# Kernel tuning notes

Measured on AMD Instinct MI355X. Metric: run time of the kernel, lower is better.

## Reference

```python
import jax, jax.numpy as jnp
import numpy as np

B, N, C = 8, 512, 256
HID_E = 32          # edge_pred hidden width
FILTERS = (64, 64, 64)
OUT = 2


def setup_inputs() -> dict:
    key = jax.random.key(0)
    ks = jax.random.split(key, 12)
    s = 0.05
    inp = {
        "x": jax.random.normal(ks[0], (B, N, C), jnp.float32),
        "A": jax.random.uniform(ks[1], (B, N, N), jnp.float32),
        "mask": jnp.ones((B, N), jnp.float32),
        # edge predictor: Linear(2C,32) -> ReLU -> Linear(32,1)
        "ew1": jax.random.normal(ks[2], (2 * C, HID_E), jnp.float32) * s,
        "eb1": jnp.zeros((HID_E,), jnp.float32),
        "ew2": jax.random.normal(ks[3], (HID_E, 1), jnp.float32) * s,
        "eb2": jnp.zeros((1,), jnp.float32),
        # GraphConv stack: Linear(in*n_relations, f) per layer (n_relations=2)
        "gw0": jax.random.normal(ks[4], (2 * C, FILTERS[0]), jnp.float32) * s,
        "gb0": jnp.zeros((FILTERS[0],), jnp.float32),
        "gw1": jax.random.normal(ks[5], (2 * FILTERS[0], FILTERS[1]), jnp.float32) * s,
        "gb1": jnp.zeros((FILTERS[1],), jnp.float32),
        "gw2": jax.random.normal(ks[6], (2 * FILTERS[1], FILTERS[2]), jnp.float32) * s,
        "gb2": jnp.zeros((FILTERS[2],), jnp.float32),
        # final classifier (dropout is identity in eval)
        "fcw": jax.random.normal(ks[7], (FILTERS[2], OUT), jnp.float32) * s,
        "fcb": jnp.zeros((OUT,), jnp.float32),
    }
    return inp


def _laplacian(A):
    # A_hat = A + I ; L = D^-1/2 A_hat D^-1/2 with D from row-sums (dim 1)
    n = A.shape[-1]
    A_hat = A + jnp.eye(n, dtype=A.dtype)
    D = (A_hat.sum(axis=1) + 1e-5) ** -0.5  # [B,N]
    return D[:, :, None] * A_hat * D[:, None, :]


def reference(x, A, mask, ew1, eb1, ew2, eb2, gw0, gb0, gw1, gb1, gw2, gb2, fcw, fcb):
    b, n, c = x.shape
    # edge MLP over all node pairs; first layer split so we never build [B,N,N,2C]
    wa, wb = ew1[:c], ew1[c:]
    xa = x @ wa  # [B,N,32] contribution of node i
    xb = x @ wb  # [B,N,32] contribution of node j
    h = jax.nn.relu(xa[:, :, None, :] + xb[:, None, :, :] + eb1)  # [B,N,N,32]
    e = (h @ ew2)[..., 0] + eb2[0]  # e[b,i,j] = edge_pred([x_i, x_j])
    # symmetrized score: exp(0.5 * (f(i,j) + f(j,i)))
    y = jnp.exp(0.5 * (e + jnp.swapaxes(e, 1, 2)))
    triu = jnp.triu(jnp.ones((n, n), bool), 1)
    valid = (mask[:, :, None] > 0) & (mask[:, None, :] > 0)
    A_pred = jnp.where(triu[None] & valid, y, 0.0)
    A_pred = A_pred + jnp.swapaxes(A_pred, 1, 2)

    # multi-relation GCN stack (relations: input A, predicted A_pred)
    L0 = _laplacian(A)
    L1 = _laplacian(A_pred)
    m = mask[:, :, None]
    h0 = x
    for W, bias in ((gw0, gb0), (gw1, gb1), (gw2, gb2)):
        xh = jnp.concatenate([L0 @ h0, L1 @ h0], axis=-1)  # [B,N,2*f_in]
        h0 = jax.nn.relu((xh @ W + bias) * m)
    g = h0.max(axis=1)  # [B, filters[-1]] global max pool over nodes
    return g @ fcw + fcb  # [B, OUT]
```

## Files before the change

kernel.cpp:

```cpp
#include <hip/hip_runtime.h>
#include <hip/hip_bf16.h>
#include <math.h>

#define NB 8
#define NN 512
#define NC 256
#define HID 32

typedef __attribute__((ext_vector_type(8))) short short8;
typedef __attribute__((ext_vector_type(4))) float float4v;
typedef unsigned short ushort_t;

__device__ __forceinline__ ushort_t f2bf(float x) {
    unsigned u = __float_as_uint(x);
    return (ushort_t)((u + 0x7fffu + ((u >> 16) & 1u)) >> 16);
}
__device__ __forceinline__ float bf2f(ushort_t h) {
    return __uint_as_float(((unsigned)h) << 16);
}

__global__ __launch_bounds__(256) void front_gemms(
    const float* __restrict__ x, const float* __restrict__ ew1,
    const float* __restrict__ eb1, const float* __restrict__ gw0,
    const float* __restrict__ A, ushort_t* __restrict__ Ah,
    float* __restrict__ xab, ushort_t* __restrict__ T0,
    float* __restrict__ dsum, unsigned* __restrict__ gmax, int* __restrict__ done)
{
    __shared__ __align__(16) union {
        struct { float sX[2][32][17]; float sW[2][32][68]; } a;
        struct { float sH[2][32][17]; float sW[2][32][132]; ushort_t sTh[128][24]; } b;
    } u;
    __shared__ float sCol[4][64];
    int t = threadIdx.x;

    if (blockIdx.x < 256) {
        if (blockIdx.x < 16) dsum[(NB * NN) + blockIdx.x * 256 + t] = 0.f;
        if (blockIdx.x == 16) {
            gmax[t] = 0u; gmax[t + 256] = 0u;
            if (t < NB) done[t] = 0;
        }
        int r0 = blockIdx.x * 16;
        int tx = t & 15, ty = t >> 4;
        int xk = (t & 15) * 2, xr = t >> 4;
        int c4 = (t & 15) * 4;
        int whalf = c4 >> 5, wcc = c4 & 31;
        float acc[4] = {0.f, 0.f, 0.f, 0.f};

        float2 rx = *(const float2*)(x + (size_t)(r0 + xr) * NC + xk);
        float4 rw0 = *(const float4*)(ew1 + (size_t)(whalf * NC + xr) * HID + wcc);
        float4 rw1 = *(const float4*)(ew1 + (size_t)(whalf * NC + xr + 16) * HID + wcc);

        for (int k0 = 0; k0 < NC; k0 += 32) {
            int cur = (k0 >> 5) & 1;
            u.a.sX[cur][xk][xr] = rx.x; u.a.sX[cur][xk + 1][xr] = rx.y;
            *(float4*)&u.a.sW[cur][xr][c4] = rw0;
            *(float4*)&u.a.sW[cur][xr + 16][c4] = rw1;
            if (k0 + 32 < NC) {
                rx  = *(const float2*)(x + (size_t)(r0 + xr) * NC + k0 + 32 + xk);
                rw0 = *(const float4*)(ew1 + (size_t)(whalf * NC + k0 + 32 + xr) * HID + wcc);
                rw1 = *(const float4*)(ew1 + (size_t)(whalf * NC + k0 + 32 + xr + 16) * HID + wcc);
            }
            __syncthreads();
#pragma unroll
            for (int k = 0; k < 32; ++k) {
                float a = u.a.sX[cur][k][ty];
                float4 w = *(const float4*)&u.a.sW[cur][k][tx * 4];
                acc[0] = fmaf(a, w.x, acc[0]); acc[1] = fmaf(a, w.y, acc[1]);
                acc[2] = fmaf(a, w.z, acc[2]); acc[3] = fmaf(a, w.w, acc[3]);
            }
        }
        int oc4 = tx * 4;
        float4 o; o.x = acc[0]; o.y = acc[1]; o.z = acc[2]; o.w = acc[3];
        if (oc4 >= 32) {
            o.x += eb1[oc4 - 32]; o.y += eb1[oc4 - 31];
            o.z += eb1[oc4 - 30]; o.w += eb1[oc4 - 29];
        }
        *(float4*)&xab[(size_t)(r0 + ty) * 64 + oc4] = o;
    } else if (blockIdx.x < 512) {
        int r0 = (blockIdx.x - 256) * 16;
        int tx = t & 31, ty = t >> 5;
        int xk = (t & 15) * 2, xr = t >> 4;
        int c4w = (t & 31) * 4;
        int whalf = c4w >> 6, wcc = c4w & 63;
        int wk = t >> 5;
        float acc0[4] = {0.f, 0.f, 0.f, 0.f};
        float acc1[4] = {0.f, 0.f, 0.f, 0.f};

        float2 rx = *(const float2*)(x + (size_t)(r0 + xr) * NC + xk);
        float4 rw[4];
#pragma unroll
        for (int rr = 0; rr < 4; ++rr)
            rw[rr] = *(const float4*)(gw0 + (size_t)(whalf * NC + wk + rr * 8) * 64 + wcc);

        for (int k0 = 0; k0 < NC; k0 += 32) {
            int cur = (k0 >> 5) & 1;
            u.b.sH[cur][xk][xr] = rx.x; u.b.sH[cur][xk + 1][xr] = rx.y;
#pragma unroll
            for (int rr = 0; rr < 4; ++rr)
                *(float4*)&u.b.sW[cur][wk + rr * 8][c4w] = rw[rr];
            if (k0 + 32 < NC) {
                rx = *(const float2*)(x + (size_t)(r0 + xr) * NC + k0 + 32 + xk);
#pragma unroll
                for (int rr = 0; rr < 4; ++rr)
                    rw[rr] = *(const float4*)(gw0 + (size_t)(whalf * NC + k0 + 32 + wk + rr * 8) * 64 + wcc);
            }
            __syncthreads();
#pragma unroll
            for (int k = 0; k < 32; ++k) {
                float a0 = u.b.sH[cur][k][ty * 2];
                float a1 = u.b.sH[cur][k][ty * 2 + 1];
                float4 w = *(const float4*)&u.b.sW[cur][k][tx * 4];
                acc0[0] = fmaf(a0, w.x, acc0[0]); acc0[1] = fmaf(a0, w.y, acc0[1]);
                acc0[2] = fmaf(a0, w.z, acc0[2]); acc0[3] = fmaf(a0, w.w, acc0[3]);
                acc1[0] = fmaf(a1, w.x, acc1[0]); acc1[1] = fmaf(a1, w.y, acc1[1]);
                acc1[2] = fmaf(a1, w.z, acc1[2]); acc1[3] = fmaf(a1, w.w, acc1[3]);
            }
        }
        __syncthreads();
        int c4 = tx * 4;
#pragma unroll
        for (int r = 0; r < 2; ++r) {
            int rl = ty * 2 + r;
            float* ap = (r == 0) ? acc0 : acc1;
#pragma unroll
            for (int n = 0; n < 4; ++n)
                u.b.sTh[c4 + n][rl] = f2bf(ap[n]);
        }
        __syncthreads();
        {
            int c = t & 127, half = t >> 7;
            int bb = r0 >> 9, ibase = r0 & (NN - 1);
            ushort_t* dst = T0 + ((size_t)(bb * 128 + c)) * NN + ibase + half * 8;
            *(short8*)dst = *(const short8*)&u.b.sTh[c][half * 8];
        }
    } else {
        int c = blockIdx.x - 512;
        int b = c >> 3, q = c & 7;
        int col = q * 64 + (t & 63);
        int r0 = t >> 6;
        const float* Ab = A + (size_t)b * NN * NN;
        ushort_t* Hb = Ah + (size_t)b * NN * NN;
        float s = 0.f;
        for (int it = 0; it < 128; ++it) {
            int row = r0 + 4 * it;
            float a = Ab[(size_t)row * NN + col];
            Hb[(size_t)row * NN + col] = f2bf(a);
            s += a;
        }
        sCol[r0][t & 63] = s;
        __syncthreads();
        if (t < 64)
            dsum[b * NN + q * 64 + t] =
                sCol[0][t] + sCol[1][t] + sCol[2][t] + sCol[3][t];
    }
}

__global__ __launch_bounds__(256) void edge_scores(
    const float* __restrict__ xab, const float* __restrict__ ew2,
    const float* __restrict__ eb2, const float* __restrict__ mask,
    ushort_t* __restrict__ APh, float* __restrict__ dsum)
{
    __shared__ __align__(16) float sI[32][68], sJ[32][68];
    __shared__ float sV[32][33];
    int b = blockIdx.z;
    int p = blockIdx.x;
    int X = 0;
    while ((X + 1) * 16 - ((X + 1) * X) / 2 <= p) ++X;
    int Y = X + (p - (X * 16 - (X * (X - 1)) / 2));
    int i0 = X * 32, j0 = Y * 32;
    int t = threadIdx.x;
    int tj = t & 31;

    float4 rW[8];
#pragma unroll
    for (int k4 = 0; k4 < 8; ++k4) rW[k4] = *(const float4*)(ew2 + k4 * 4);
    float eb2v = eb2[0];

    {
        int c4 = (t & 15) * 4;
#pragma unroll
        for (int rr = 0; rr < 2; ++rr) {
            int r = (t >> 4) + rr * 16;
            float4 vi = *(const float4*)(xab + ((size_t)(b * NN + i0 + r)) * 64 + c4);
            float4 vj = *(const float4*)(xab + ((size_t)(b * NN + j0 + r)) * 64 + c4);
            *(float4*)&sI[r][c4] = vi;
            *(float4*)&sJ[r][c4] = vj;
        }
    }
    __syncthreads();

    float rJlo[32], rJhi[32];
#pragma unroll
    for (int k4 = 0; k4 < 8; ++k4) {
        float4 a4 = *(const float4*)&sJ[tj][k4 * 4];
        float4 b4 = *(const float4*)&sJ[tj][32 + k4 * 4];
        rJlo[k4 * 4 + 0] = a4.x; rJlo[k4 * 4 + 1] = a4.y;
        rJlo[k4 * 4 + 2] = a4.z; rJlo[k4 * 4 + 3] = a4.w;
        rJhi[k4 * 4 + 0] = b4.x; rJhi[k4 * 4 + 1] = b4.y;
        rJhi[k4 * 4 + 2] = b4.z; rJhi[k4 * 4 + 3] = b4.w;
    }
    float mj = mask[b * NN + j0 + tj];

#pragma unroll
    for (int pz = 0; pz < 4; ++pz) {
        int ti = (t >> 5) + pz * 8;
        float sij = 0.f, sji = 0.f;
#pragma unroll
        for (int k4 = 0; k4 < 8; ++k4) {
            float4 ia = *(const float4*)&sI[ti][k4 * 4];
            float4 ib = *(const float4*)&sI[ti][32 + k4 * 4];
            float4 wv = rW[k4];
            sij = fmaf(fmaxf(ia.x + rJhi[k4 * 4 + 0], 0.f), wv.x, sij);
            sji = fmaf(fmaxf(rJlo[k4 * 4 + 0] + ib.x, 0.f), wv.x, sji);
            sij = fmaf(fmaxf(ia.y + rJhi[k4 * 4 + 1], 0.f), wv.y, sij);
            sji = fmaf(fmaxf(rJlo[k4 * 4 + 1] + ib.y, 0.f), wv.y, sji);
            sij = fmaf(fmaxf(ia.z + rJhi[k4 * 4 + 2], 0.f), wv.z, sij);
            sji = fmaf(fmaxf(rJlo[k4 * 4 + 2] + ib.z, 0.f), wv.z, sji);
            sij = fmaf(fmaxf(ia.w + rJhi[k4 * 4 + 3], 0.f), wv.w, sij);
            sji = fmaf(fmaxf(rJlo[k4 * 4 + 3] + ib.w, 0.f), wv.w, sji);
        }
        int i = i0 + ti, j = j0 + tj;
        bool ok = (i != j) && (mask[b * NN + i] > 0.f) && (mj > 0.f);
        sV[ti][tj] = ok ? expf(0.5f * (sij + sji) + eb2v) : 0.f;
    }
    __syncthreads();
#pragma unroll
    for (int pz = 0; pz < 4; ++pz) {
        int r = (t >> 5) + pz * 8, c = t & 31;
        size_t o1 = ((size_t)(b * NN + i0 + r)) * NN + j0 + c;
        size_t o2 = ((size_t)(b * NN + j0 + r)) * NN + i0 + c;
        APh[o1] = f2bf(sV[r][c]);
        APh[o2] = f2bf(sV[c][r]);
    }
    if (t < 32) {
        float s = 0.f;
#pragma unroll
        for (int r = 0; r < 32; ++r) s += sV[r][t];
        atomicAdd(&dsum[(NB * NN) + b * NN + j0 + t], s);
    } else if (t < 64 && X != Y) {
        int c = t - 32;
        float s = 0.f;
#pragma unroll
        for (int j = 0; j < 32; ++j) s += sV[c][j];
        atomicAdd(&dsum[(NB * NN) + b * NN + i0 + c], s);
    }
}

__global__ __launch_bounds__(256) void fused_layer(
    const ushort_t* __restrict__ Ah, const ushort_t* __restrict__ APh,
    const ushort_t* __restrict__ Pa, const ushort_t* __restrict__ Pb,
    ushort_t* __restrict__ Qa, ushort_t* __restrict__ Qb,
    const float* __restrict__ dsum, const float* __restrict__ gb,
    const float* __restrict__ mask, const float* __restrict__ gwN,
    unsigned* __restrict__ gmax, int* __restrict__ done,
    const float* __restrict__ fcw, const float* __restrict__ fcb,
    float* __restrict__ out, int dualP, int mode, int scaleP)
{
    __shared__ union {
        struct {
            ushort_t sA[2][2][16][72];
            ushort_t sP1[2][64][72];
            ushort_t sP2[2][64][72];
        } a;
        struct { ushort_t sWT[128][40]; } b;
    } u;
    __shared__ float sRed[2][32][17];
    __shared__ float sH16[16][36];
    __shared__ float sD[2][16];
    __shared__ __align__(16) float sDj[2][NN];
    __shared__ int lastFlag;

    int t = threadIdx.x;
    int b = blockIdx.z, ch = blockIdx.y, i0 = blockIdx.x * 16;
    int lane = t & 63, w = t >> 6;
    int quad = lane >> 4, m16 = lane & 15;
    int lap = w >> 1, cg = w & 1;

    if (scaleP) {
#pragma unroll
        for (int s = 0; s < 4; ++s) {
            int idx = t + s * 256;
            int lp = idx >> 9, j = idx & (NN - 1);
            sDj[lp][j] = rsqrtf(dsum[lp * (NB * NN) + b * NN + j] + 1.0f + 1e-5f);
        }
    }

    int sa_arr = t >> 7, sa_id = t & 127;
    int sa_r = sa_id >> 3, sa_q = sa_id & 7;
    const ushort_t* sa_src = (sa_arr ? APh : Ah)
        + ((size_t)(b * NN + i0 + sa_r)) * NN + sa_q * 8;
    int pl0 = t >> 3, pq = t & 7;
    size_t poff0 = ((size_t)(b * 128 + ch * 32 + pl0)) * NN + pq * 8;
    size_t poff1 = ((size_t)(b * 128 + 64 + ch * 32 + pl0)) * NN + pq * 8;

    int gi = b * NN + i0 + m16;
    float dspre = dsum[lap * (NB * NN) + gi];
    int cbase = cg * 16 + quad * 4;
    size_t pvbase = ((size_t)(b * 128 + lap * 64 + ch * 32 + cbase)) * NN + i0 + m16;
    ushort_t pvA[4], pvB[4];
#pragma unroll
    for (int r = 0; r < 4; ++r) {
        pvA[r] = Pa[pvbase + (size_t)r * NN];
        pvB[r] = dualP ? Pb[pvbase + (size_t)r * NN] : (ushort_t)0;
    }

    float gwPre[16];
    if (mode == 0) {
#pragma unroll
        for (int kk = 0; kk < 8; ++kk) {
            int chunk = t + kk * 256;
            int c = chunk & 127;
            int k = (chunk >> 7) * 2;
            int base = (c < 64) ? (ch * 32) : (64 + ch * 32);
            int gc = c & 63;
            gwPre[kk * 2]     = gwN[(size_t)(base + k) * 64 + gc];
            gwPre[kk * 2 + 1] = gwN[(size_t)(base + k + 1) * 64 + gc];
        }
    }

    float4v acc = {0.f, 0.f, 0.f, 0.f};

    short8 A0, P1a0, P1b0, P2a0, P2b0;
    short8 A1, P1a1, P1b1, P2a1, P2b1;

    A0   = *(const short8*)(sa_src);
    P1a0 = *(const short8*)(Pa + poff0);
    P1b0 = *(const short8*)(Pa + poff1);
    A1   = *(const short8*)(sa_src + 64);
    P1a1 = *(const short8*)(Pa + poff0 + 64);
    P1b1 = *(const short8*)(Pa + poff1 + 64);
    P2a0 = P1a0; P2b0 = P1b0; P2a1 = P1a1; P2b1 = P1b1;
    if (dualP) {
        P2a0 = *(const short8*)(Pb + poff0);
        P2b0 = *(const short8*)(Pb + poff1);
        P2a1 = *(const short8*)(Pb + poff0 + 64);
        P2b1 = *(const short8*)(Pb + poff1 + 64);
    }
    __syncthreads();

#pragma unroll
    for (int i = 0; i < 8; ++i) {
        int k0 = i * 64;
        int cur = i & 1;
        short8 rA   = cur ? A1   : A0;
        short8 rP1a = cur ? P1a1 : P1a0;
        short8 rP1b = cur ? P1b1 : P1b0;
        short8 rP2a = cur ? P2a1 : P2a0;
        short8 rP2b = cur ? P2b1 : P2b0;

        *(short8*)&u.a.sA[cur][sa_arr][sa_r][sa_q * 8] = rA;
        if (scaleP) {
            float4v d0a = *(const float4v*)&sDj[0][k0 + pq * 8];
            float4v d0b = *(const float4v*)&sDj[0][k0 + pq * 8 + 4];
            float4v d1a = *(const float4v*)&sDj[1][k0 + pq * 8];
            float4v d1b = *(const float4v*)&sDj[1][k0 + pq * 8 + 4];
            short8 w0, w1;
#pragma unroll
            for (int e = 0; e < 4; ++e) {
                w0[e]     = (short)f2bf(bf2f((ushort_t)rP1a[e])     * d0a[e]);
                w0[e + 4] = (short)f2bf(bf2f((ushort_t)rP1a[e + 4]) * d0b[e]);
                w1[e]     = (short)f2bf(bf2f((ushort_t)rP1b[e])     * d1a[e]);
                w1[e + 4] = (short)f2bf(bf2f((ushort_t)rP1b[e + 4]) * d1b[e]);
            }
            *(short8*)&u.a.sP1[cur][pl0][pq * 8] = w0;
            *(short8*)&u.a.sP1[cur][32 + pl0][pq * 8] = w1;
        } else {
            *(short8*)&u.a.sP1[cur][pl0][pq * 8] = rP1a;
            *(short8*)&u.a.sP1[cur][32 + pl0][pq * 8] = rP1b;
            if (dualP) {
                *(short8*)&u.a.sP2[cur][pl0][pq * 8] = rP2a;
                *(short8*)&u.a.sP2[cur][32 + pl0][pq * 8] = rP2b;
            }
        }
        if (i + 2 < 8) {
            int kn = k0 + 128;
            if (cur == 0) {
                A0   = *(const short8*)(sa_src + kn);
                P1a0 = *(const short8*)(Pa + poff0 + kn);
                P1b0 = *(const short8*)(Pa + poff1 + kn);
                if (dualP) {
                    P2a0 = *(const short8*)(Pb + poff0 + kn);
                    P2b0 = *(const short8*)(Pb + poff1 + kn);
                }
            } else {
                A1   = *(const short8*)(sa_src + kn);
                P1a1 = *(const short8*)(Pa + poff0 + kn);
                P1b1 = *(const short8*)(Pa + poff1 + kn);
                if (dualP) {
                    P2a1 = *(const short8*)(Pb + poff0 + kn);
                    P2b1 = *(const short8*)(Pb + poff1 + kn);
                }
            }
        }
        __syncthreads();
#pragma unroll
        for (int kh = 0; kh < 2; ++kh) {
            int ko = kh * 32 + quad * 8;
            short8 av = *(const short8*)&u.a.sA[cur][lap][m16][ko];
            short8 p1 = *(const short8*)&u.a.sP1[cur][w * 16 + m16][ko];
            acc = __builtin_amdgcn_mfma_f32_16x16x32_bf16(p1, av, acc, 0, 0, 0);
            if (dualP) {
                short8 p2 = *(const short8*)&u.a.sP2[cur][w * 16 + m16][ko];
                acc = __builtin_amdgcn_mfma_f32_16x16x32_bf16(p2, av, acc, 0, 0, 0);
            }
        }
    }
    float d = rsqrtf(dspre + 1.0f + 1e-5f);
    if (cg == 0 && quad == 0) sD[lap][m16] = d;
#pragma unroll
    for (int r = 0; r < 4; ++r) {
        int c32 = cbase + r;
        float pv = bf2f(pvA[r]);
        if (dualP) pv += bf2f(pvB[r]);
        if (scaleP) pv *= d;
        sRed[lap][c32][m16] = d * (acc[r] + pv);
    }
    __syncthreads();
#pragma unroll
    for (int s = 0; s < 2; ++s) {
        int idx = t + s * 256;
        int c32 = idx & 31, i = idx >> 5;
        float mv = mask[b * NN + i0 + i];
        float v = (sRed[0][c32][i] + sRed[1][c32][i] + gb[ch * 32 + c32]) * mv;
        sH16[i][c32] = fmaxf(v, 0.f);
    }
    __syncthreads();

    if (mode == 0) {
#pragma unroll
        for (int kk = 0; kk < 8; ++kk) {
            int chunk = t + kk * 256;
            int c = chunk & 127;
            int k = (chunk >> 7) * 2;
            unsigned pk = (unsigned)f2bf(gwPre[kk * 2])
                        | ((unsigned)f2bf(gwPre[kk * 2 + 1]) << 16);
            *(unsigned*)&u.b.sWT[c][k] = pk;
        }
        __syncthreads();
        float4 h0 = *(const float4*)&sH16[m16][quad * 8];
        float4 h1 = *(const float4*)&sH16[m16][quad * 8 + 4];
        short8 bfv;
        bfv[0] = f2bf(h0.x); bfv[1] = f2bf(h0.y); bfv[2] = f2bf(h0.z); bfv[3] = f2bf(h0.w);
        bfv[4] = f2bf(h1.x); bfv[5] = f2bf(h1.y); bfv[6] = f2bf(h1.z); bfv[7] = f2bf(h1.w);
        ushort_t* Q = ch ? Qb : Qa;
#pragma unroll
        for (int s2 = 0; s2 < 2; ++s2) {
            int ctile = w * 2 + s2;
            short8 af = *(const short8*)&u.b.sWT[ctile * 16 + m16][quad * 8];
            float4v dacc = {0.f, 0.f, 0.f, 0.f};
            dacc = __builtin_amdgcn_mfma_f32_16x16x32_bf16(af, bfv, dacc, 0, 0, 0);
            float dsc = sD[(ctile >= 4) ? 1 : 0][m16];
#pragma unroll
            for (int r = 0; r < 4; ++r) {
                int c = ctile * 16 + quad * 4 + r;
                Q[((size_t)(b * 128 + c)) * NN + i0 + m16] = f2bf(dsc * dacc[r]);
            }
        }
    } else {
        if (t < 32) {
            float mx = 0.f;
#pragma unroll
            for (int r = 0; r < 16; ++r) mx = fmaxf(mx, sH16[r][t]);
            atomicMax(&gmax[b * 64 + ch * 32 + t], __float_as_uint(mx));
        }
        __syncthreads();
        if (t == 0) {
            __threadfence();
            int old = atomicAdd(&done[b], 1);
            lastFlag = (old == 63);
        }
        __syncthreads();
        if (lastFlag) {
            if (t < 64) {
                unsigned ub = __hip_atomic_load(&gmax[b * 64 + t],
                                                __ATOMIC_RELAXED,
                                                __HIP_MEMORY_SCOPE_AGENT);
                ((float*)sRed)[t] = __uint_as_float(ub);
            }
            __syncthreads();
            if (t < 2) {
                float a2 = fcb[t];
#pragma unroll
                for (int k = 0; k < 64; ++k)
                    a2 = fmaf(((float*)sRed)[k], fcw[k * 2 + t], a2);
                out[b * 2 + t] = a2;
            }
        }
    }
}

extern "C" void kernel_launch(void* const* d_in, const int* in_sizes, int n_in,
                              void* d_out, int out_size, void* d_ws, size_t ws_size,
                              hipStream_t stream)
{
    const float* x    = (const float*)d_in[0];
    const float* A    = (const float*)d_in[1];
    const float* mask = (const float*)d_in[2];
    const float* ew1  = (const float*)d_in[3];
    const float* eb1  = (const float*)d_in[4];
    const float* ew2  = (const float*)d_in[5];
    const float* eb2  = (const float*)d_in[6];
    const float* gw0  = (const float*)d_in[7];
    const float* gb0  = (const float*)d_in[8];
    const float* gw1  = (const float*)d_in[9];
    const float* gb1  = (const float*)d_in[10];
    const float* gw2  = (const float*)d_in[11];
    const float* gb2  = (const float*)d_in[12];
    const float* fcw  = (const float*)d_in[13];
    const float* fcb  = (const float*)d_in[14];
    float* out = (float*)d_out;
    char* ws = (char*)d_ws;

    const size_t NEL = (size_t)NB * NN * NN;
    const size_t PSL = (size_t)NB * 128 * NN;
    float*    xab  = (float*)ws;                   ws += 262144 * 4;
    ushort_t* APh  = (ushort_t*)ws;                ws += NEL * 2;
    ushort_t* Ahs  = (ushort_t*)ws;                ws += NEL * 2;
    float*    dsum = (float*)ws;                   ws += 8192 * 4;
    ushort_t* PT_A = (ushort_t*)ws;                ws += PSL * 2;
    ushort_t* PB1a = (ushort_t*)ws;                ws += PSL * 2;
    ushort_t* PB1b = (ushort_t*)ws;                ws += PSL * 2;
    ushort_t* PB2a = (ushort_t*)ws;                ws += PSL * 2;
    ushort_t* PB2b = (ushort_t*)ws;                ws += PSL * 2;
    unsigned* gmax = (unsigned*)ws;                ws += 512 * 4;
    int*      done = (int*)ws;                     ws += 64 * 4;

    front_gemms<<<576, 256, 0, stream>>>(x, ew1, eb1, gw0, A, Ahs, xab, PT_A,
                                         dsum, gmax, done);
    edge_scores<<<dim3(136, 1, NB), 256, 0, stream>>>(xab, ew2, eb2, mask,
                                                      APh, dsum);

    fused_layer<<<dim3(32, 2, NB), 256, 0, stream>>>(
        Ahs, APh, PT_A, PT_A, PB1a, PB1b, dsum, gb0, mask, gw1,
        gmax, done, fcw, fcb, out, 0, 0, 1);
    fused_layer<<<dim3(32, 2, NB), 256, 0, stream>>>(
        Ahs, APh, PB1a, PB1b, PB2a, PB2b, dsum, gb1, mask, gw2,
        gmax, done, fcw, fcb, out, 1, 0, 0);
    fused_layer<<<dim3(32, 2, NB), 256, 0, stream>>>(
        Ahs, APh, PB2a, PB2b, PB2a, PB2b, dsum, gb2, mask, gw2,
        gmax, done, fcw, fcb, out, 1, 1, 0);
}
```

Measured before the change: 151.2 us.

## Rebalance front kernels so edge scoring runs alongside gw0 GEMM and A conversion

Splits the first kernel so only the xa/xb GEMM (which edge scoring depends on) runs first. The gw0 GEMM, the A-to-bf16 conversion with row sums, and the edge scoring now share one launch of 1408 blocks. The independent work can then overlap instead of sitting behind a dependency boundary. The gw0 GEMM also drops its double-buffered shared memory for a single buffer with an extra barrier, which shrinks the LDS union but serialises load and compute within that path.

```diff
diff --git a/kernel.cpp b/kernel.cpp
--- a/kernel.cpp
+++ b/kernel.cpp
@@ -19,65 +19,76 @@
     return __uint_as_float(((unsigned)h) << 16);
 }
 
-__global__ __launch_bounds__(256) void front_gemms(
+__global__ __launch_bounds__(256) void xaxb_gemm(
     const float* __restrict__ x, const float* __restrict__ ew1,
-    const float* __restrict__ eb1, const float* __restrict__ gw0,
-    const float* __restrict__ A, ushort_t* __restrict__ Ah,
-    float* __restrict__ xab, ushort_t* __restrict__ T0,
+    const float* __restrict__ eb1, float* __restrict__ xab,
     float* __restrict__ dsum, unsigned* __restrict__ gmax, int* __restrict__ done)
 {
+    __shared__ __align__(16) struct { float sX[2][32][17]; float sW[2][32][68]; } u;
+    int t = threadIdx.x;
+
+    if (blockIdx.x < 16) dsum[(NB * NN) + blockIdx.x * 256 + t] = 0.f;
+    if (blockIdx.x == 16) {
+        gmax[t] = 0u; gmax[t + 256] = 0u;
+        if (t < NB) done[t] = 0;
+    }
+    int r0 = blockIdx.x * 16;
+    int tx = t & 15, ty = t >> 4;
+    int xk = (t & 15) * 2, xr = t >> 4;
+    int c4 = (t & 15) * 4;
+    int whalf = c4 >> 5, wcc = c4 & 31;
+    float acc[4] = {0.f, 0.f, 0.f, 0.f};
+
+    float2 rx = *(const float2*)(x + (size_t)(r0 + xr) * NC + xk);
+    float4 rw0 = *(const float4*)(ew1 + (size_t)(whalf * NC + xr) * HID + wcc);
+    float4 rw1 = *(const float4*)(ew1 + (size_t)(whalf * NC + xr + 16) * HID + wcc);
+
+    for (int k0 = 0; k0 < NC; k0 += 32) {
+        int cur = (k0 >> 5) & 1;
+        u.sX[cur][xk][xr] = rx.x; u.sX[cur][xk + 1][xr] = rx.y;
+        *(float4*)&u.sW[cur][xr][c4] = rw0;
+        *(float4*)&u.sW[cur][xr + 16][c4] = rw1;
+        if (k0 + 32 < NC) {
+            rx  = *(const float2*)(x + (size_t)(r0 + xr) * NC + k0 + 32 + xk);
+            rw0 = *(const float4*)(ew1 + (size_t)(whalf * NC + k0 + 32 + xr) * HID + wcc);
+            rw1 = *(const float4*)(ew1 + (size_t)(whalf * NC + k0 + 32 + xr + 16) * HID + wcc);
+        }
+        __syncthreads();
+#pragma unroll
+        for (int k = 0; k < 32; ++k) {
+            float a = u.sX[cur][k][ty];
+            float4 w = *(const float4*)&u.sW[cur][k][tx * 4];
+            acc[0] = fmaf(a, w.x, acc[0]); acc[1] = fmaf(a, w.y, acc[1]);
+            acc[2] = fmaf(a, w.z, acc[2]); acc[3] = fmaf(a, w.w, acc[3]);
+        }
+    }
+    int oc4 = tx * 4;
+    float4 o; o.x = acc[0]; o.y = acc[1]; o.z = acc[2]; o.w = acc[3];
+    if (oc4 >= 32) {
+        o.x += eb1[oc4 - 32]; o.y += eb1[oc4 - 31];
+        o.z += eb1[oc4 - 30]; o.w += eb1[oc4 - 29];
+    }
+    *(float4*)&xab[(size_t)(r0 + ty) * 64 + oc4] = o;
+}
+
+__global__ __launch_bounds__(256) void edge_plus(
+    const float* __restrict__ x, const float* __restrict__ gw0,
+    const float* __restrict__ A, ushort_t* __restrict__ Ah,
+    const float* __restrict__ xab, const float* __restrict__ ew2,
+    const float* __restrict__ eb2, const float* __restrict__ mask,
+    ushort_t* __restrict__ T0, ushort_t* __restrict__ APh,
+    float* __restrict__ dsum)
+{
     __shared__ __align__(16) union {
-        struct { float sX[2][32][17]; float sW[2][32][68]; } a;
-        struct { float sH[2][32][17]; float sW[2][32][132]; ushort_t sTh[128][24]; } b;
+        struct { float sH[32][17]; float sW[32][132]; ushort_t sTh[128][24]; } b;
+        struct { float sI[32][68]; float sJ[32][68]; float sV[32][33]; } e;
     } u;
     __shared__ float sCol[4][64];
+    int bid = blockIdx.x;
     int t = threadIdx.x;
 
-    if (blockIdx.x < 256) {
-        if (blockIdx.x < 16) dsum[(NB * NN) + blockIdx.x * 256 + t] = 0.f;
-        if (blockIdx.x == 16) {
-            gmax[t] = 0u; gmax[t + 256] = 0u;
-            if (t < NB) done[t] = 0;
-        }
-        int r0 = blockIdx.x * 16;
-        int tx = t & 15, ty = t >> 4;
-        int xk = (t & 15) * 2, xr = t >> 4;
-        int c4 = (t & 15) * 4;
-        int whalf = c4 >> 5, wcc = c4 & 31;
-        float acc[4] = {0.f, 0.f, 0.f, 0.f};
-
-        float2 rx = *(const float2*)(x + (size_t)(r0 + xr) * NC + xk);
-        float4 rw0 = *(const float4*)(ew1 + (size_t)(whalf * NC + xr) * HID + wcc);
-        float4 rw1 = *(const float4*)(ew1 + (size_t)(whalf * NC + xr + 16) * HID + wcc);
-
-        for (int k0 = 0; k0 < NC; k0 += 32) {
-            int cur = (k0 >> 5) & 1;
-            u.a.sX[cur][xk][xr] = rx.x; u.a.sX[cur][xk + 1][xr] = rx.y;
-            *(float4*)&u.a.sW[cur][xr][c4] = rw0;
-            *(float4*)&u.a.sW[cur][xr + 16][c4] = rw1;
-            if (k0 + 32 < NC) {
-                rx  = *(const float2*)(x + (size_t)(r0 + xr) * NC + k0 + 32 + xk);
-                rw0 = *(const float4*)(ew1 + (size_t)(whalf * NC + k0 + 32 + xr) * HID + wcc);
-                rw1 = *(const float4*)(ew1 + (size_t)(whalf * NC + k0 + 32 + xr + 16) * HID + wcc);
-            }
-            __syncthreads();
-#pragma unroll
-            for (int k = 0; k < 32; ++k) {
-                float a = u.a.sX[cur][k][ty];
-                float4 w = *(const float4*)&u.a.sW[cur][k][tx * 4];
-                acc[0] = fmaf(a, w.x, acc[0]); acc[1] = fmaf(a, w.y, acc[1]);
-                acc[2] = fmaf(a, w.z, acc[2]); acc[3] = fmaf(a, w.w, acc[3]);
-            }
-        }
-        int oc4 = tx * 4;
-        float4 o; o.x = acc[0]; o.y = acc[1]; o.z = acc[2]; o.w = acc[3];
-        if (oc4 >= 32) {
-            o.x += eb1[oc4 - 32]; o.y += eb1[oc4 - 31];
-            o.z += eb1[oc4 - 30]; o.w += eb1[oc4 - 29];
-        }
-        *(float4*)&xab[(size_t)(r0 + ty) * 64 + oc4] = o;
-    } else if (blockIdx.x < 512) {
-        int r0 = (blockIdx.x - 256) * 16;
+    if (bid < 256) {
+        int r0 = bid * 16;
         int tx = t & 31, ty = t >> 5;
         int xk = (t & 15) * 2, xr = t >> 4;
         int c4w = (t & 31) * 4;
@@ -93,11 +104,10 @@
             rw[rr] = *(const float4*)(gw0 + (size_t)(whalf * NC + wk + rr * 8) * 64 + wcc);
 
         for (int k0 = 0; k0 < NC; k0 += 32) {
-            int cur = (k0 >> 5) & 1;
-            u.b.sH[cur][xk][xr] = rx.x; u.b.sH[cur][xk + 1][xr] = rx.y;
+            u.b.sH[xk][xr] = rx.x; u.b.sH[xk + 1][xr] = rx.y;
 #pragma unroll
             for (int rr = 0; rr < 4; ++rr)
-                *(float4*)&u.b.sW[cur][wk + rr * 8][c4w] = rw[rr];
+                *(float4*)&u.b.sW[wk + rr * 8][c4w] = rw[rr];
             if (k0 + 32 < NC) {
                 rx = *(const float2*)(x + (size_t)(r0 + xr) * NC + k0 + 32 + xk);
 #pragma unroll
@@ -107,16 +117,16 @@
             __syncthreads();
 #pragma unroll
             for (int k = 0; k < 32; ++k) {
-                float a0 = u.b.sH[cur][k][ty * 2];
-                float a1 = u.b.sH[cur][k][ty * 2 + 1];
-                float4 w = *(const float4*)&u.b.sW[cur][k][tx * 4];
+                float a0 = u.b.sH[k][ty * 2];
+                float a1 = u.b.sH[k][ty * 2 + 1];
+                float4 w = *(const float4*)&u.b.sW[k][tx * 4];
                 acc0[0] = fmaf(a0, w.x, acc0[0]); acc0[1] = fmaf(a0, w.y, acc0[1]);
                 acc0[2] = fmaf(a0, w.z, acc0[2]); acc0[3] = fmaf(a0, w.w, acc0[3]);
                 acc1[0] = fmaf(a1, w.x, acc1[0]); acc1[1] = fmaf(a1, w.y, acc1[1]);
                 acc1[2] = fmaf(a1, w.z, acc1[2]); acc1[3] = fmaf(a1, w.w, acc1[3]);
             }
-        }
-        __syncthreads();
+            __syncthreads();
+        }
         int c4 = tx * 4;
 #pragma unroll
         for (int r = 0; r < 2; ++r) {
@@ -133,8 +143,8 @@
             ushort_t* dst = T0 + ((size_t)(bb * 128 + c)) * NN + ibase + half * 8;
             *(short8*)dst = *(const short8*)&u.b.sTh[c][half * 8];
         }
-    } else {
-        int c = blockIdx.x - 512;
+    } else if (bid < 320) {
+        int c = bid - 256;
         int b = c >> 3, q = c & 7;
         int col = q * 64 + (t & 63);
         int r0 = t >> 6;
@@ -152,97 +162,88 @@
         if (t < 64)
             dsum[b * NN + q * 64 + t] =
                 sCol[0][t] + sCol[1][t] + sCol[2][t] + sCol[3][t];
-    }
-}
-
-__global__ __launch_bounds__(256) void edge_scores(
-    const float* __restrict__ xab, const float* __restrict__ ew2,
-    const float* __restrict__ eb2, const float* __restrict__ mask,
-    ushort_t* __restrict__ APh, float* __restrict__ dsum)
-{
-    __shared__ __align__(16) float sI[32][68], sJ[32][68];
-    __shared__ float sV[32][33];
-    int b = blockIdx.z;
-    int p = blockIdx.x;
-    int X = 0;
-    while ((X + 1) * 16 - ((X + 1) * X) / 2 <= p) ++X;
-    int Y = X + (p - (X * 16 - (X * (X - 1)) / 2));
-    int i0 = X * 32, j0 = Y * 32;
-    int t = threadIdx.x;
-    int tj = t & 31;
-
-    float4 rW[8];
-#pragma unroll
-    for (int k4 = 0; k4 < 8; ++k4) rW[k4] = *(const float4*)(ew2 + k4 * 4);
-    float eb2v = eb2[0];
-
-    {
-        int c4 = (t & 15) * 4;
-#pragma unroll
-        for (int rr = 0; rr < 2; ++rr) {
-            int r = (t >> 4) + rr * 16;
-            float4 vi = *(const float4*)(xab + ((size_t)(b * NN + i0 + r)) * 64 + c4);
-            float4 vj = *(const float4*)(xab + ((size_t)(b * NN + j0 + r)) * 64 + c4);
-            *(float4*)&sI[r][c4] = vi;
-            *(float4*)&sJ[r][c4] = vj;
-        }
-    }
-    __syncthreads();
-
-    float rJlo[32], rJhi[32];
-#pragma unroll
-    for (int k4 = 0; k4 < 8; ++k4) {
-        float4 a4 = *(const float4*)&sJ[tj][k4 * 4];
-        float4 b4 = *(const float4*)&sJ[tj][32 + k4 * 4];
-        rJlo[k4 * 4 + 0] = a4.x; rJlo[k4 * 4 + 1] = a4.y;
-        rJlo[k4 * 4 + 2] = a4.z; rJlo[k4 * 4 + 3] = a4.w;
-        rJhi[k4 * 4 + 0] = b4.x; rJhi[k4 * 4 + 1] = b4.y;
-        rJhi[k4 * 4 + 2] = b4.z; rJhi[k4 * 4 + 3] = b4.w;
-    }
-    float mj = mask[b * NN + j0 + tj];
-
-#pragma unroll
-    for (int pz = 0; pz < 4; ++pz) {
-        int ti = (t >> 5) + pz * 8;
-        float sij = 0.f, sji = 0.f;
+    } else {
+        int e0 = bid - 320;
+        int b = e0 / 136, p = e0 - b * 136;
+        int X = 0;
+        while ((X + 1) * 16 - ((X + 1) * X) / 2 <= p) ++X;
+        int Y = X + (p - (X * 16 - (X * (X - 1)) / 2));
+        int i0 = X * 32, j0 = Y * 32;
+        int tj = t & 31;
+
+        float4 rW[8];
+#pragma unroll
+        for (int k4 = 0; k4 < 8; ++k4) rW[k4] = *(const float4*)(ew2 + k4 * 4);
+        float eb2v = eb2[0];
+
+        {
+            int c4 = (t & 15) * 4;
+#pragma unroll
+            for (int rr = 0; rr < 2; ++rr) {
+                int r = (t >> 4) + rr * 16;
+                float4 vi = *(const float4*)(xab + ((size_t)(b * NN + i0 + r)) * 64 + c4);
+                float4 vj = *(const float4*)(xab + ((size_t)(b * NN + j0 + r)) * 64 + c4);
+                *(float4*)&u.e.sI[r][c4] = vi;
+                *(float4*)&u.e.sJ[r][c4] = vj;
+            }
+        }
+        __syncthreads();
+
+        float rJlo[32], rJhi[32];
 #pragma unroll
         for (int k4 = 0; k4 < 8; ++k4) {
-            float4 ia = *(const float4*)&sI[ti][k4 * 4];
-            float4 ib = *(const float4*)&sI[ti][32 + k4 * 4];
-            float4 wv = rW[k4];
-            sij = fmaf(fmaxf(ia.x + rJhi[k4 * 4 + 0], 0.f), wv.x, sij);
-            sji = fmaf(fmaxf(rJlo[k4 * 4 + 0] + ib.x, 0.f), wv.x, sji);
-            sij = fmaf(fmaxf(ia.y + rJhi[k4 * 4 + 1], 0.f), wv.y, sij);
-            sji = fmaf(fmaxf(rJlo[k4 * 4 + 1] + ib.y, 0.f), wv.y, sji);
-            sij = fmaf(fmaxf(ia.z + rJhi[k4 * 4 + 2], 0.f), wv.z, sij);
-            sji = fmaf(fmaxf(rJlo[k4 * 4 + 2] + ib.z, 0.f), wv.z, sji);
-            sij = fmaf(fmaxf(ia.w + rJhi[k4 * 4 + 3], 0.f), wv.w, sij);
-            sji = fmaf(fmaxf(rJlo[k4 * 4 + 3] + ib.w, 0.f), wv.w, sji);
-        }
-        int i = i0 + ti, j = j0 + tj;
-        bool ok = (i != j) && (mask[b * NN + i] > 0.f) && (mj > 0.f);
-        sV[ti][tj] = ok ? expf(0.5f * (sij + sji) + eb2v) : 0.f;
-    }
-    __syncthreads();
-#pragma unroll
-    for (int pz = 0; pz < 4; ++pz) {
-        int r = (t >> 5) + pz * 8, c = t & 31;
-        size_t o1 = ((size_t)(b * NN + i0 + r)) * NN + j0 + c;
-        size_t o2 = ((size_t)(b * NN + j0 + r)) * NN + i0 + c;
-        APh[o1] = f2bf(sV[r][c]);
-        APh[o2] = f2bf(sV[c][r]);
-    }
-    if (t < 32) {
-        float s = 0.f;
-#pragma unroll
-        for (int r = 0; r < 32; ++r) s += sV[r][t];
-        atomicAdd(&dsum[(NB * NN) + b * NN + j0 + t], s);
-    } else if (t < 64 && X != Y) {
-        int c = t - 32;
-        float s = 0.f;
-#pragma unroll
-        for (int j = 0; j < 32; ++j) s += sV[c][j];
-        atomicAdd(&dsum[(NB * NN) + b * NN + i0 + c], s);
+            float4 a4 = *(const float4*)&u.e.sJ[tj][k4 * 4];
+            float4 b4 = *(const float4*)&u.e.sJ[tj][32 + k4 * 4];
+            rJlo[k4 * 4 + 0] = a4.x; rJlo[k4 * 4 + 1] = a4.y;
+            rJlo[k4 * 4 + 2] = a4.z; rJlo[k4 * 4 + 3] = a4.w;
+            rJhi[k4 * 4 + 0] = b4.x; rJhi[k4 * 4 + 1] = b4.y;
+            rJhi[k4 * 4 + 2] = b4.z; rJhi[k4 * 4 + 3] = b4.w;
+        }
+        float mj = mask[b * NN + j0 + tj];
+
+#pragma unroll
+        for (int pz = 0; pz < 4; ++pz) {
+            int ti = (t >> 5) + pz * 8;
+            float sij = 0.f, sji = 0.f;
+#pragma unroll
+            for (int k4 = 0; k4 < 8; ++k4) {
+                float4 ia = *(const float4*)&u.e.sI[ti][k4 * 4];
+                float4 ib = *(const float4*)&u.e.sI[ti][32 + k4 * 4];
+                float4 wv = rW[k4];
+                sij = fmaf(fmaxf(ia.x + rJhi[k4 * 4 + 0], 0.f), wv.x, sij);
+                sji = fmaf(fmaxf(rJlo[k4 * 4 + 0] + ib.x, 0.f), wv.x, sji);
+                sij = fmaf(fmaxf(ia.y + rJhi[k4 * 4 + 1], 0.f), wv.y, sij);
+                sji = fmaf(fmaxf(rJlo[k4 * 4 + 1] + ib.y, 0.f), wv.y, sji);
+                sij = fmaf(fmaxf(ia.z + rJhi[k4 * 4 + 2], 0.f), wv.z, sij);
+                sji = fmaf(fmaxf(rJlo[k4 * 4 + 2] + ib.z, 0.f), wv.z, sji);
+                sij = fmaf(fmaxf(ia.w + rJhi[k4 * 4 + 3], 0.f), wv.w, sij);
+                sji = fmaf(fmaxf(rJlo[k4 * 4 + 3] + ib.w, 0.f), wv.w, sji);
+            }
+            int i = i0 + ti, j = j0 + tj;
+            bool ok = (i != j) && (mask[b * NN + i] > 0.f) && (mj > 0.f);
+            u.e.sV[ti][tj] = ok ? expf(0.5f * (sij + sji) + eb2v) : 0.f;
+        }
+        __syncthreads();
+#pragma unroll
+        for (int pz = 0; pz < 4; ++pz) {
+            int r = (t >> 5) + pz * 8, c = t & 31;
+            size_t o1 = ((size_t)(b * NN + i0 + r)) * NN + j0 + c;
+            size_t o2 = ((size_t)(b * NN + j0 + r)) * NN + i0 + c;
+            APh[o1] = f2bf(u.e.sV[r][c]);
+            APh[o2] = f2bf(u.e.sV[c][r]);
+        }
+        if (t < 32) {
+            float s = 0.f;
+#pragma unroll
+            for (int r = 0; r < 32; ++r) s += u.e.sV[r][t];
+            atomicAdd(&dsum[(NB * NN) + b * NN + j0 + t], s);
+        } else if (t < 64 && X != Y) {
+            int c = t - 32;
+            float s = 0.f;
+#pragma unroll
+            for (int j = 0; j < 32; ++j) s += u.e.sV[c][j];
+            atomicAdd(&dsum[(NB * NN) + b * NN + i0 + c], s);
+        }
     }
 }
 
@@ -525,10 +526,9 @@
     unsigned* gmax = (unsigned*)ws;                ws += 512 * 4;
     int*      done = (int*)ws;                     ws += 64 * 4;
 
-    front_gemms<<<576, 256, 0, stream>>>(x, ew1, eb1, gw0, A, Ahs, xab, PT_A,
-                                         dsum, gmax, done);
-    edge_scores<<<dim3(136, 1, NB), 256, 0, stream>>>(xab, ew2, eb2, mask,
-                                                      APh, dsum);
+    xaxb_gemm<<<256, 256, 0, stream>>>(x, ew1, eb1, xab, dsum, gmax, done);
+    edge_plus<<<1408, 256, 0, stream>>>(x, gw0, A, Ahs, xab, ew2, eb2, mask,
+                                        PT_A, APh, dsum);
 
     fused_layer<<<dim3(32, 2, NB), 256, 0, stream>>>(
         Ahs, APh, PT_A, PT_A, PB1a, PB1b, dsum, gb0, mask, gw1,
```

Measured after the change: 149.6 us. About the same (-1.1%).
